# Kernel optimization log

Hardware: AMD Instinct MI355X
Metric: run time of the kernel (lower is better)

The kernel has to match this reference:

```python
import jax, jax.numpy as jnp
import numpy as np

N = 116                      # AAL atlas nodes
E = N * (N - 1) // 2         # 6670 edges of the fully connected connectome
HID = 64
EDIM = 5
OUT = 4
ENC = HID + N // 2           # 122 raw brain-encoding features
EPS = 1e-10


def setup_inputs() -> dict:
    key = jax.random.key(0)
    ks = jax.random.split(key, 15)
    iu = np.triu_indices(N, k=1)                      # matches torch.nonzero(triu) order
    edge_index = jnp.asarray(np.stack(iu), dtype=jnp.int32)   # [2, E]
    rn = lambda k, s, sc=0.1: jax.random.normal(k, s, dtype=jnp.float32) * sc
    return dict(
        encoding_raw=rn(ks[0], (N, ENC), 1.0),
        edge_attr=rn(ks[1], (E, EDIM), 1.0),
        edge_index=edge_index,
        W_enc=rn(ks[2], (ENC, HID)), b_enc=rn(ks[3], (HID,)),
        W1=rn(ks[4], (HID, HID)), b1=rn(ks[5], (HID,)), p1=rn(ks[6], (1, EDIM)),
        We=rn(ks[7], (EDIM, EDIM)), be=rn(ks[8], (EDIM,)), pe=rn(ks[9], (1, HID)),
        W2=rn(ks[10], (HID, HID)), b2=rn(ks[11], (HID,)), p2=rn(ks[12], (1, EDIM)),
        Wl=rn(ks[13], (HID, OUT)), bl=rn(ks[14], (OUT,)),
    )


def _forward(encoding_raw, edge_attr, edge_index, W_enc, b_enc,
             W1, b1, p1, We, be, pe, W2, b2, p2, Wl, bl):
    eye_n = jnp.eye(N, dtype=jnp.float32)
    eye_e = jnp.eye(E, dtype=jnp.float32)
    adj_v = 1.0 - eye_n          # fully-connected node adjacency, zero diagonal
    adj_e = 1.0 - eye_e          # edge adjacency: ones minus eye
    # Incidence matrix T [N, E]: T[i,e] = T[j,e] = 1 for edge e = (i, j)
    cols = jnp.arange(E)
    T = (jnp.zeros((N, E), dtype=jnp.float32)
         .at[edge_index[0], cols].set(1.0)
         .at[edge_index[1], cols].set(1.0))

    # BrainEncoding: x = Linear(raw encoding)  (batch.x is None -> x = encodings)
    x = encoding_raw @ W_enc + b_enc                    # [N, HID]

    def node_conv(Hv, He, W, b, p):
        d = (He @ p.T)[:, 0]                            # [E] learned scalar per edge
        mult = (T * d) @ T.T                            # T diag(d) T^T  -> [N, N]
        # M1 = eye*1 + (1-eye)*mult, then * adj_v (zero diag) => mult * adj_v
        A = mult * adj_v
        return A @ (Hv @ W) + b

    def edge_conv(Hv, He, W, b, p):
        dv = (Hv @ p.T)[:, 0]                           # [N] learned scalar per node
        mult = T.T @ (dv[:, None] * T)                  # T^T diag(dv) T -> [E, E] dense
        A = mult * adj_e                                # M3 * adj_e => zero diag, off-diag mult
        A = A / (A.max(axis=0, keepdims=True) + EPS)    # column-max normalization
        return A @ (He @ W) + b

    # node_conv1 -> relu (dropout is identity in eval)
    x = jax.nn.relu(node_conv(x, edge_attr, W1, b1, p1))
    e = jax.nn.relu(edge_attr)
    # edge_conv1 -> relu
    e = jax.nn.relu(edge_conv(x, e, We, be, pe))
    x = jax.nn.relu(x)                                  # relu applied again (idempotent)
    # node_conv2 (no relu after)
    x = node_conv(x, e, W2, b2, p2)
    # global mean pool over the single graph, then classifier head
    pooled = jnp.mean(x, axis=0, keepdims=True)         # [1, HID]
    return pooled @ Wl + bl                             # [1, OUT]


def reference(encoding_raw, edge_attr, edge_index, W_enc, b_enc,
              W1, b1, p1, We, be, pe, W2, b2, p2, Wl, bl):
    return _forward(encoding_raw, edge_attr, edge_index, W_enc, b_enc,
                    W1, b1, p1, We, be, pe, W2, b2, p2, Wl, bl)
```

## Files before the change

### kernel.cpp

```cpp
#include <hip/hip_runtime.h>


#define NN   116
#define EE   6670
#define HID  64
#define EDIM 5
#define OUTD 4
#define ENC  122
#define EPSF 1e-10f
#define NH   (NN*HID)

__device__ __forceinline__ int eid_ij(int i, int j) {
    int a = i < j ? i : j;
    int b = i < j ? j : i;
    return a*NN - ((a*(a+1)) >> 1) + (b - a - 1);
}

__global__ __launch_bounds__(256) void kA(
    const float* __restrict__ enc, const float* __restrict__ ea,
    const float* __restrict__ W_enc, const float* __restrict__ b_enc,
    const float* __restrict__ p1, const float* __restrict__ We,
    const float* __restrict__ W1,
    float* __restrict__ Y1, float* __restrict__ d1, float* __restrict__ G)
{
    const int tid = threadIdx.x;
    if (blockIdx.x < 29) {
        __shared__ __align__(16) float sWe[ENC*HID];
        __shared__ __align__(16) float sW1[HID*HID];
        __shared__ __align__(16) float sEnc[4*ENC];
        __shared__ float sX[4*HID];
        {
            const float4* g4 = (const float4*)W_enc; float4* s4 = (float4*)sWe;
            for (int u = tid; u < ENC*HID/4; u += 256) s4[u] = g4[u];
        }
        {
            const float4* g4 = (const float4*)W1; float4* s4 = (float4*)sW1;
            for (int u = tid; u < HID*HID/4; u += 256) s4[u] = g4[u];
        }
        {
            const float4* g4 = (const float4*)(enc + blockIdx.x*4*ENC);
            float4* s4 = (float4*)sEnc;
            for (int u = tid; u < 4*ENC/4; u += 256) s4[u] = g4[u];
        }
        __syncthreads();
        const int w = tid >> 6, h = tid & 63;
        const int i = blockIdx.x*4 + w;
        float acc = b_enc[h];
        const float* er = sEnc + w*ENC;
        #pragma unroll 4
        for (int k = 0; k < ENC; ++k) acc = fmaf(er[k], sWe[k*HID + h], acc);
        sX[w*HID + h] = acc;
        __syncthreads();
        float a2 = 0.f;
        const float* xr = sX + w*HID;
        #pragma unroll 8
        for (int k = 0; k < HID; ++k) a2 = fmaf(xr[k], sW1[k*HID + h], a2);
        Y1[i*HID + h] = a2;
    } else {
        int u = (blockIdx.x - 29)*256 + tid;
        if (u < EE) {
            const float* r = ea + u*EDIM;
            float a0 = 0.f;
            #pragma unroll
            for (int k = 0; k < EDIM; ++k) a0 = fmaf(r[k], p1[k], a0);
            d1[u] = a0;
        } else if (u < EE + EE*EDIM) {
            int idx = u - EE;
            int e = idx / EDIM, k = idx - e*EDIM;
            const float* r = ea + e*EDIM;
            float a0 = 0.f;
            #pragma unroll
            for (int m = 0; m < EDIM; ++m) a0 = fmaf(fmaxf(r[m], 0.f), We[m*EDIM + k], a0);
            G[idx] = a0;
        }
    }
}

__global__ __launch_bounds__(256) void kB(
    const float* __restrict__ d1, const float* __restrict__ Y1,
    const float* __restrict__ b1, const float* __restrict__ pe,
    const float* __restrict__ W2,
    float* __restrict__ dv, float* __restrict__ Y2,
    float* __restrict__ P, int* __restrict__ cnt)
{
    __shared__ __align__(16) float sY[NH];
    __shared__ __align__(16) float sD[EE];
    __shared__ float sX2[4*HID];
    const int tid = threadIdx.x;
    if (blockIdx.x == 0) {
        if (tid < HID) P[tid] = 0.f;
        if (tid == 0) *cnt = 0;
    }
    {
        const float4* g4 = (const float4*)Y1; float4* s4 = (float4*)sY;
        for (int u = tid; u < NH/4; u += 256) s4[u] = g4[u];
        const float2* g2 = (const float2*)d1; float2* s2 = (float2*)sD;
        for (int u = tid; u < EE/2; u += 256) s2[u] = g2[u];
    }
    __syncthreads();
    const int w = tid >> 6, h = tid & 63;
    const int i = blockIdx.x*4 + w;
    float acc = b1[h];
    #pragma unroll 4
    for (int j = 0; j < NN; ++j) {
        int jj = (j == i) ? (j ^ 1) : j;
        float wgt = (j == i) ? 0.f : sD[eid_ij(i, jj)];
        acc = fmaf(wgt, sY[jj*HID + h], acc);
    }
    float v = fmaxf(acc, 0.f);
    float r = v * pe[h];
    #pragma unroll
    for (int off = 32; off > 0; off >>= 1) r += __shfl_down(r, off, 64);
    if (h == 0) dv[i] = r;
    sX2[w*HID + h] = v;
    __syncthreads();
    float a2 = 0.f;
    const float* xr = sX2 + w*HID;
    #pragma unroll 8
    for (int k = 0; k < HID; ++k) a2 = fmaf(xr[k], W2[k*HID + h], a2);
    Y2[i*HID + h] = a2;
}

__global__ __launch_bounds__(256) void kC(
    const float* __restrict__ G, const float* __restrict__ dv,
    float* __restrict__ S)
{
    const int wg = blockIdx.x*4 + (threadIdx.x >> 6);
    const int lane = threadIdx.x & 63;
    const int i = wg / EDIM, k = wg - i*EDIM;
    const float di = dv[i];
    float acc = 0.f;
    #pragma unroll
    for (int rep = 0; rep < 2; ++rep) {
        int j = lane + rep*64;
        if (j < NN && j != i) {
            float cm = fmaxf(fmaxf(di, dv[j]), 0.f) + EPSF;
            acc += G[eid_ij(i, j)*EDIM + k] / cm;
        }
    }
    #pragma unroll
    for (int off = 32; off > 0; off >>= 1) acc += __shfl_down(acc, off, 64);
    if (lane == 0) S[wg] = acc;
}

__global__ __launch_bounds__(256) void kDEF(
    const float* __restrict__ G, const float* __restrict__ dvg,
    const float* __restrict__ Sg, const float* __restrict__ Y2,
    const float* __restrict__ be, const float* __restrict__ p2,
    const float* __restrict__ b2, const float* __restrict__ Wl,
    const float* __restrict__ bl,
    float* __restrict__ P, int* __restrict__ cnt, float* __restrict__ out)
{
    __shared__ __align__(16) float sY[NH];
    __shared__ float sS[NN*EDIM];
    __shared__ float sDv[NN];
    __shared__ float sD2[4*NN];
    __shared__ float sR[4*HID];
    __shared__ int sLast;
    const int tid = threadIdx.x;
    const int wid = tid >> 6, lane = tid & 63;

    float ber[EDIM], p2r[EDIM];
    #pragma unroll
    for (int k = 0; k < EDIM; ++k) { ber[k] = be[k]; p2r[k] = p2[k]; }

    {
        const float4* g4 = (const float4*)Y2; float4* s4 = (float4*)sY;
        for (int u = tid; u < NH/4; u += 256) s4[u] = g4[u];
    }
    for (int u = tid; u < NN*EDIM; u += 256) sS[u] = Sg[u];
    if (tid < NN) sDv[tid] = dvg[tid];
    __syncthreads();

    {
        const int i = blockIdx.x*4 + wid;
        #pragma unroll
        for (int rep = 0; rep < 2; ++rep) {
            const int j = lane + rep*64;
            if (j < NN) {
                float val = 0.f;
                if (j != i) {
                    const int a = i < j ? i : j, b = i < j ? j : i;
                    const int e = a*NN - ((a*(a+1)) >> 1) + (b - a - 1);
                    const float da = sDv[a], db = sDv[b];
                    const float rc = 1.f / (fmaxf(fmaxf(da, db), 0.f) + EPSF);
                    #pragma unroll
                    for (int k = 0; k < EDIM; ++k) {
                        const float gp = G[e*EDIM + k] * rc;
                        const float v = fmaf(da, sS[a*EDIM + k] - gp,
                                       fmaf(db, sS[b*EDIM + k] - gp, ber[k]));
                        val = fmaf(fmaxf(v, 0.f), p2r[k], val);
                    }
                }
                sD2[wid*NN + j] = val;
            }
        }
    }
    __syncthreads();

    {
        float acc = b2[lane];
        const float* d2r = sD2 + wid*NN;
        #pragma unroll 4
        for (int j = 0; j < NN; ++j)
            acc = fmaf(d2r[j], sY[j*HID + lane], acc);
        sR[wid*HID + lane] = acc;
    }
    __syncthreads();
    if (wid == 0) {
        float s4 = sR[lane] + sR[HID + lane] + sR[2*HID + lane] + sR[3*HID + lane];
        atomicAdd(&P[lane], s4);
    }
    __syncthreads();

    if (tid == 0) {
        __threadfence();
        int old = __hip_atomic_fetch_add(cnt, 1, __ATOMIC_ACQ_REL, __HIP_MEMORY_SCOPE_AGENT);
        sLast = (old == 28) ? 1 : 0;
    }
    __syncthreads();
    if (sLast && wid == 0) {
        const float pv = __hip_atomic_load(&P[lane], __ATOMIC_ACQUIRE, __HIP_MEMORY_SCOPE_AGENT);
        const float val = pv * (1.0f / NN);
        float res[OUTD];
        #pragma unroll
        for (int o = 0; o < OUTD; ++o) {
            float r = val * Wl[lane*OUTD + o];
            #pragma unroll
            for (int off = 32; off > 0; off >>= 1) r += __shfl_xor(r, off, 64);
            res[o] = r;
        }
        if (lane < OUTD) out[lane] = res[lane] + bl[lane];
    }
}

extern "C" void kernel_launch(void* const* d_in, const int* in_sizes, int n_in,
                              void* d_out, int out_size, void* d_ws, size_t ws_size,
                              hipStream_t stream)
{
    const float* enc   = (const float*)d_in[0];
    const float* ea    = (const float*)d_in[1];
    const float* W_enc = (const float*)d_in[3];
    const float* b_enc = (const float*)d_in[4];
    const float* W1    = (const float*)d_in[5];
    const float* b1    = (const float*)d_in[6];
    const float* p1    = (const float*)d_in[7];
    const float* We    = (const float*)d_in[8];
    const float* be    = (const float*)d_in[9];
    const float* pe    = (const float*)d_in[10];
    const float* W2    = (const float*)d_in[11];
    const float* b2    = (const float*)d_in[12];
    const float* p2    = (const float*)d_in[13];
    const float* Wl    = (const float*)d_in[14];
    const float* bl    = (const float*)d_in[15];
    float* ws = (float*)d_ws;

    float* Y1 = ws;
    float* Y2 = ws + NH;
    float* d1 = ws + 2*NH;
    float* G  = d1 + EE;
    float* dv = G + EE*EDIM;
    float* S  = dv + NN;
    float* P  = S + NN*EDIM;
    int*  cnt = (int*)(P + HID);
    float* out = (float*)d_out;

    kA<<<29 + (EE + EE*EDIM + 255)/256, 256, 0, stream>>>(enc, ea, W_enc, b_enc, p1, We, W1, Y1, d1, G);
    kB<<<29, 256, 0, stream>>>(d1, Y1, b1, pe, W2, dv, Y2, P, cnt);
    kC<<<(NN*EDIM)/4, 256, 0, stream>>>(G, dv, S);
    kDEF<<<29, 256, 0, stream>>>(G, dv, S, Y2, be, p2, b2, Wl, bl, P, cnt, out);
}
```

Before: 116.7 us.

## Drop shared-memory staging and read weights from global; one thread per edge in kA

After: 134.5 us. +15.2%, slower.

```diff
diff --git a/kernel.cpp b/kernel.cpp
--- a/kernel.cpp
+++ b/kernel.cpp
@@ -25,53 +25,38 @@
 {
     const int tid = threadIdx.x;
     if (blockIdx.x < 29) {
-        __shared__ __align__(16) float sWe[ENC*HID];
-        __shared__ __align__(16) float sW1[HID*HID];
-        __shared__ __align__(16) float sEnc[4*ENC];
         __shared__ float sX[4*HID];
-        {
-            const float4* g4 = (const float4*)W_enc; float4* s4 = (float4*)sWe;
-            for (int u = tid; u < ENC*HID/4; u += 256) s4[u] = g4[u];
-        }
-        {
-            const float4* g4 = (const float4*)W1; float4* s4 = (float4*)sW1;
-            for (int u = tid; u < HID*HID/4; u += 256) s4[u] = g4[u];
-        }
-        {
-            const float4* g4 = (const float4*)(enc + blockIdx.x*4*ENC);
-            float4* s4 = (float4*)sEnc;
-            for (int u = tid; u < 4*ENC/4; u += 256) s4[u] = g4[u];
-        }
-        __syncthreads();
         const int w = tid >> 6, h = tid & 63;
         const int i = blockIdx.x*4 + w;
+        const float* er = enc + i*ENC;
         float acc = b_enc[h];
-        const float* er = sEnc + w*ENC;
         #pragma unroll 4
-        for (int k = 0; k < ENC; ++k) acc = fmaf(er[k], sWe[k*HID + h], acc);
+        for (int k = 0; k < ENC; ++k) acc = fmaf(er[k], W_enc[k*HID + h], acc);
         sX[w*HID + h] = acc;
         __syncthreads();
         float a2 = 0.f;
         const float* xr = sX + w*HID;
         #pragma unroll 8
-        for (int k = 0; k < HID; ++k) a2 = fmaf(xr[k], sW1[k*HID + h], a2);
+        for (int k = 0; k < HID; ++k) a2 = fmaf(xr[k], W1[k*HID + h], a2);
         Y1[i*HID + h] = a2;
     } else {
-        int u = (blockIdx.x - 29)*256 + tid;
-        if (u < EE) {
-            const float* r = ea + u*EDIM;
+        const int e = (blockIdx.x - 29)*256 + tid;
+        if (e < EE) {
+            const float* r = ea + e*EDIM;
+            float rv[EDIM];
+            #pragma unroll
+            for (int m = 0; m < EDIM; ++m) rv[m] = r[m];
             float a0 = 0.f;
             #pragma unroll
-            for (int k = 0; k < EDIM; ++k) a0 = fmaf(r[k], p1[k], a0);
-            d1[u] = a0;
-        } else if (u < EE + EE*EDIM) {
-            int idx = u - EE;
-            int e = idx / EDIM, k = idx - e*EDIM;
-            const float* r = ea + e*EDIM;
-            float a0 = 0.f;
-            #pragma unroll
-            for (int m = 0; m < EDIM; ++m) a0 = fmaf(fmaxf(r[m], 0.f), We[m*EDIM + k], a0);
-            G[idx] = a0;
+            for (int k = 0; k < EDIM; ++k) a0 = fmaf(rv[k], p1[k], a0);
+            d1[e] = a0;
+            #pragma unroll
+            for (int k = 0; k < EDIM; ++k) {
+                float g = 0.f;
+                #pragma unroll
+                for (int m = 0; m < EDIM; ++m) g = fmaf(fmaxf(rv[m], 0.f), We[m*EDIM + k], g);
+                G[e*EDIM + k] = g;
+            }
         }
     }
 }
@@ -83,29 +68,20 @@
     float* __restrict__ dv, float* __restrict__ Y2,
     float* __restrict__ P, int* __restrict__ cnt)
 {
-    __shared__ __align__(16) float sY[NH];
-    __shared__ __align__(16) float sD[EE];
     __shared__ float sX2[4*HID];
     const int tid = threadIdx.x;
     if (blockIdx.x == 0) {
         if (tid < HID) P[tid] = 0.f;
         if (tid == 0) *cnt = 0;
     }
-    {
-        const float4* g4 = (const float4*)Y1; float4* s4 = (float4*)sY;
-        for (int u = tid; u < NH/4; u += 256) s4[u] = g4[u];
-        const float2* g2 = (const float2*)d1; float2* s2 = (float2*)sD;
-        for (int u = tid; u < EE/2; u += 256) s2[u] = g2[u];
-    }
-    __syncthreads();
     const int w = tid >> 6, h = tid & 63;
     const int i = blockIdx.x*4 + w;
     float acc = b1[h];
     #pragma unroll 4
     for (int j = 0; j < NN; ++j) {
         int jj = (j == i) ? (j ^ 1) : j;
-        float wgt = (j == i) ? 0.f : sD[eid_ij(i, jj)];
-        acc = fmaf(wgt, sY[jj*HID + h], acc);
+        float wgt = (j == i) ? 0.f : d1[eid_ij(i, jj)];
+        acc = fmaf(wgt, Y1[jj*HID + h], acc);
     }
     float v = fmaxf(acc, 0.f);
     float r = v * pe[h];
@@ -151,7 +127,6 @@
     const float* __restrict__ bl,
     float* __restrict__ P, int* __restrict__ cnt, float* __restrict__ out)
 {
-    __shared__ __align__(16) float sY[NH];
     __shared__ float sS[NN*EDIM];
     __shared__ float sDv[NN];
     __shared__ float sD2[4*NN];
@@ -164,10 +139,6 @@
     #pragma unroll
     for (int k = 0; k < EDIM; ++k) { ber[k] = be[k]; p2r[k] = p2[k]; }
 
-    {
-        const float4* g4 = (const float4*)Y2; float4* s4 = (float4*)sY;
-        for (int u = tid; u < NH/4; u += 256) s4[u] = g4[u];
-    }
     for (int u = tid; u < NN*EDIM; u += 256) sS[u] = Sg[u];
     if (tid < NN) sDv[tid] = dvg[tid];
     __syncthreads();
@@ -203,7 +174,7 @@
         const float* d2r = sD2 + wid*NN;
         #pragma unroll 4
         for (int j = 0; j < NN; ++j)
-            acc = fmaf(d2r[j], sY[j*HID + lane], acc);
+            acc = fmaf(d2r[j], Y2[j*HID + lane], acc);
         sR[wid*HID + lane] = acc;
     }
     __syncthreads();
@@ -265,7 +236,7 @@
     int*  cnt = (int*)(P + HID);
     float* out = (float*)d_out;
 
-    kA<<<29 + (EE + EE*EDIM + 255)/256, 256, 0, stream>>>(enc, ea, W_enc, b_enc, p1, We, W1, Y1, d1, G);
+    kA<<<29 + (EE + 255)/256, 256, 0, stream>>>(enc, ea, W_enc, b_enc, p1, We, W1, Y1, d1, G);
     kB<<<29, 256, 0, stream>>>(d1, Y1, b1, pe, W2, dv, Y2, P, cnt);
     kC<<<(NN*EDIM)/4, 256, 0, stream>>>(G, dv, S);
     kDEF<<<29, 256, 0, stream>>>(G, dv, S, Y2, be, p2, b2, Wl, bl, P, cnt, out);
```

## Defer W2 projection past mean pool and merge per-edge feature work

Applied to the files above, without the earlier changes.

After: 116.2 us, median of 2. Within noise of the previous version (-0.4%).

```diff
diff --git a/kernel.cpp b/kernel.cpp
--- a/kernel.cpp
+++ b/kernel.cpp
@@ -57,21 +57,23 @@
         for (int k = 0; k < HID; ++k) a2 = fmaf(xr[k], sW1[k*HID + h], a2);
         Y1[i*HID + h] = a2;
     } else {
-        int u = (blockIdx.x - 29)*256 + tid;
-        if (u < EE) {
-            const float* r = ea + u*EDIM;
+        const int e = (blockIdx.x - 29)*256 + tid;
+        if (e < EE) {
+            const float* r = ea + e*EDIM;
+            float rv[EDIM];
+            #pragma unroll
+            for (int m = 0; m < EDIM; ++m) rv[m] = r[m];
             float a0 = 0.f;
             #pragma unroll
-            for (int k = 0; k < EDIM; ++k) a0 = fmaf(r[k], p1[k], a0);
-            d1[u] = a0;
-        } else if (u < EE + EE*EDIM) {
-            int idx = u - EE;
-            int e = idx / EDIM, k = idx - e*EDIM;
-            const float* r = ea + e*EDIM;
-            float a0 = 0.f;
-            #pragma unroll
-            for (int m = 0; m < EDIM; ++m) a0 = fmaf(fmaxf(r[m], 0.f), We[m*EDIM + k], a0);
-            G[idx] = a0;
+            for (int k = 0; k < EDIM; ++k) a0 = fmaf(rv[k], p1[k], a0);
+            d1[e] = a0;
+            #pragma unroll
+            for (int k = 0; k < EDIM; ++k) {
+                float g = 0.f;
+                #pragma unroll
+                for (int m = 0; m < EDIM; ++m) g = fmaf(fmaxf(rv[m], 0.f), We[m*EDIM + k], g);
+                G[e*EDIM + k] = g;
+            }
         }
     }
 }
@@ -79,13 +81,11 @@
 __global__ __launch_bounds__(256) void kB(
     const float* __restrict__ d1, const float* __restrict__ Y1,
     const float* __restrict__ b1, const float* __restrict__ pe,
-    const float* __restrict__ W2,
-    float* __restrict__ dv, float* __restrict__ Y2,
+    float* __restrict__ dv, float* __restrict__ x2,
     float* __restrict__ P, int* __restrict__ cnt)
 {
     __shared__ __align__(16) float sY[NH];
     __shared__ __align__(16) float sD[EE];
-    __shared__ float sX2[4*HID];
     const int tid = threadIdx.x;
     if (blockIdx.x == 0) {
         if (tid < HID) P[tid] = 0.f;
@@ -112,43 +112,44 @@
     #pragma unroll
     for (int off = 32; off > 0; off >>= 1) r += __shfl_down(r, off, 64);
     if (h == 0) dv[i] = r;
-    sX2[w*HID + h] = v;
-    __syncthreads();
-    float a2 = 0.f;
-    const float* xr = sX2 + w*HID;
-    #pragma unroll 8
-    for (int k = 0; k < HID; ++k) a2 = fmaf(xr[k], W2[k*HID + h], a2);
-    Y2[i*HID + h] = a2;
+    x2[i*HID + h] = v;
 }
 
 __global__ __launch_bounds__(256) void kC(
     const float* __restrict__ G, const float* __restrict__ dv,
     float* __restrict__ S)
 {
-    const int wg = blockIdx.x*4 + (threadIdx.x >> 6);
+    const int i = blockIdx.x*4 + (threadIdx.x >> 6);
     const int lane = threadIdx.x & 63;
-    const int i = wg / EDIM, k = wg - i*EDIM;
     const float di = dv[i];
-    float acc = 0.f;
+    float acc[EDIM] = {0.f, 0.f, 0.f, 0.f, 0.f};
     #pragma unroll
     for (int rep = 0; rep < 2; ++rep) {
-        int j = lane + rep*64;
+        const int j = lane + rep*64;
         if (j < NN && j != i) {
-            float cm = fmaxf(fmaxf(di, dv[j]), 0.f) + EPSF;
-            acc += G[eid_ij(i, j)*EDIM + k] / cm;
-        }
-    }
-    #pragma unroll
-    for (int off = 32; off > 0; off >>= 1) acc += __shfl_down(acc, off, 64);
-    if (lane == 0) S[wg] = acc;
+            const float cm = fmaxf(fmaxf(di, dv[j]), 0.f) + EPSF;
+            const float* gr = G + eid_ij(i, j)*EDIM;
+            #pragma unroll
+            for (int k = 0; k < EDIM; ++k) acc[k] += gr[k] / cm;
+        }
+    }
+    #pragma unroll
+    for (int k = 0; k < EDIM; ++k) {
+        #pragma unroll
+        for (int off = 32; off > 0; off >>= 1) acc[k] += __shfl_down(acc[k], off, 64);
+    }
+    if (lane == 0) {
+        #pragma unroll
+        for (int k = 0; k < EDIM; ++k) S[i*EDIM + k] = acc[k];
+    }
 }
 
 __global__ __launch_bounds__(256) void kDEF(
     const float* __restrict__ G, const float* __restrict__ dvg,
-    const float* __restrict__ Sg, const float* __restrict__ Y2,
+    const float* __restrict__ Sg, const float* __restrict__ x2,
     const float* __restrict__ be, const float* __restrict__ p2,
-    const float* __restrict__ b2, const float* __restrict__ Wl,
-    const float* __restrict__ bl,
+    const float* __restrict__ W2, const float* __restrict__ b2,
+    const float* __restrict__ Wl, const float* __restrict__ bl,
     float* __restrict__ P, int* __restrict__ cnt, float* __restrict__ out)
 {
     __shared__ __align__(16) float sY[NH];
@@ -165,7 +166,7 @@
     for (int k = 0; k < EDIM; ++k) { ber[k] = be[k]; p2r[k] = p2[k]; }
 
     {
-        const float4* g4 = (const float4*)Y2; float4* s4 = (float4*)sY;
+        const float4* g4 = (const float4*)x2; float4* s4 = (float4*)sY;
         for (int u = tid; u < NH/4; u += 256) s4[u] = g4[u];
     }
     for (int u = tid; u < NN*EDIM; u += 256) sS[u] = Sg[u];
@@ -199,7 +200,7 @@
     __syncthreads();
 
     {
-        float acc = b2[lane];
+        float acc = 0.f;
         const float* d2r = sD2 + wid*NN;
         #pragma unroll 4
         for (int j = 0; j < NN; ++j)
@@ -221,11 +222,15 @@
     __syncthreads();
     if (sLast && wid == 0) {
         const float pv = __hip_atomic_load(&P[lane], __ATOMIC_ACQUIRE, __HIP_MEMORY_SCOPE_AGENT);
-        const float val = pv * (1.0f / NN);
+        const float zbar = pv * (1.0f / NN);
+        float q = b2[lane];
+        #pragma unroll 8
+        for (int j = 0; j < HID; ++j)
+            q = fmaf(__shfl(zbar, j, 64), W2[j*HID + lane], q);
         float res[OUTD];
         #pragma unroll
         for (int o = 0; o < OUTD; ++o) {
-            float r = val * Wl[lane*OUTD + o];
+            float r = q * Wl[lane*OUTD + o];
             #pragma unroll
             for (int off = 32; off > 0; off >>= 1) r += __shfl_xor(r, off, 64);
             res[o] = r;
@@ -256,7 +261,7 @@
     float* ws = (float*)d_ws;
 
     float* Y1 = ws;
-    float* Y2 = ws + NH;
+    float* x2 = ws + NH;
     float* d1 = ws + 2*NH;
     float* G  = d1 + EE;
     float* dv = G + EE*EDIM;
@@ -265,8 +270,8 @@
     int*  cnt = (int*)(P + HID);
     float* out = (float*)d_out;
 
-    kA<<<29 + (EE + EE*EDIM + 255)/256, 256, 0, stream>>>(enc, ea, W_enc, b_enc, p1, We, W1, Y1, d1, G);
-    kB<<<29, 256, 0, stream>>>(d1, Y1, b1, pe, W2, dv, Y2, P, cnt);
-    kC<<<(NN*EDIM)/4, 256, 0, stream>>>(G, dv, S);
-    kDEF<<<29, 256, 0, stream>>>(G, dv, S, Y2, be, p2, b2, Wl, bl, P, cnt, out);
-}
+    kA<<<29 + (EE + 255)/256, 256, 0, stream>>>(enc, ea, W_enc, b_enc, p1, We, W1, Y1, d1, G);
+    kB<<<29, 256, 0, stream>>>(d1, Y1, b1, pe, dv, x2, P, cnt);
+    kC<<<29, 256, 0, stream>>>(G, dv, S);
+    kDEF<<<29, 256, 0, stream>>>(G, dv, S, x2, be, p2, W2, b2, Wl, bl, P, cnt, out);
+}
```
